# Optimization experiments

Measured on AMD Instinct MI355X. Metric: run time of the kernel, lower is better.

## Reference

```python
import jax, jax.numpy as jnp
import numpy as np

R, S, H, B = 50000, 8, 128, 4096

def setup_inputs() -> dict:
    key = jax.random.key(0)
    ks = jax.random.split(key, 8)
    return {
        "memory": jax.random.normal(ks[0], (R, S, H), dtype=jnp.float32) * 0.02,
        "o_emb_w": jax.random.normal(ks[1], (H,), dtype=jnp.float32),
        "o_emb_r": jax.random.normal(ks[2], (B, H), dtype=jnp.float32),
        "attn_W": jax.random.normal(ks[3], (H, H), dtype=jnp.float32) * (1.0 / np.sqrt(H)),
        "sim_w": jax.random.normal(ks[4], (2 * H, 1), dtype=jnp.float32) * 0.05,
        "sim_b": jax.random.normal(ks[5], (1,), dtype=jnp.float32) * 0.05,
        "forget_w": jax.random.normal(ks[6], (2 * H, 1), dtype=jnp.float32) * 0.05,
        "o_rg": 12345,
        "d_rg": jax.random.randint(ks[7], (B,), 0, R, dtype=jnp.int32),
    }

def reference(memory, o_emb_w, o_emb_r, attn_W, sim_w, sim_b, forget_w, o_rg, d_rg):
    h = memory.shape[-1]
    # --- write (state='w'): gather one region, sigmoid forget gate, scatter update ---
    sel = memory[o_rg]                                   # [S, H]
    o_ext = jnp.broadcast_to(o_emb_w, sel.shape)         # [S, H]
    # forget_linear(cat([o_emb, mem])) with no bias
    gate = jax.nn.sigmoid(o_ext @ forget_w[:h] + sel @ forget_w[h:])  # [S, 1]
    new_slot = sel * (1.0 - gate) + o_ext * gate
    new_mem = memory.at[o_rg].set(new_slot)              # equivalent to memory*(1-pad)+o_emb*pad
    # --- read (state='r'): gather per-batch region, concat-MLP attention over slots ---
    km = new_mem[d_rg]                                   # [B, S, H]
    q = o_emb_r @ attn_W                                 # [B, H]
    kv = km @ attn_W                                     # [B, S, H] (key == value input, same projection)
    # sim_mlp = Linear(2H,1)+ReLU applied to cat([q, k]), then softmax over slot dim
    logits = jax.nn.relu((q @ sim_w[:h])[:, None, :] + kv @ sim_w[h:] + sim_b)  # [B, S, 1]
    score = jax.nn.softmax(logits, axis=-2)              # softmax over slots
    mem_out = jnp.sum(score * kv, axis=-2)               # [B, H]
    return mem_out
```

## Files before the change

### kernel.cpp

```cpp
#include <hip/hip_runtime.h>
#include <math.h>

#define H 128
#define S 8
#define BB 4

__device__ __forceinline__ float wave_allreduce_sum(float v) {
    #pragma unroll
    for (int off = 32; off; off >>= 1) v += __shfl_xor(v, off, 64);
    return v;
}

__global__ __launch_bounds__(128) void prep_kernel(
        const float* __restrict__ memory,
        const float* __restrict__ o_emb_w,
        const float* __restrict__ attn_W,
        const float* __restrict__ sim_w,
        const float* __restrict__ forget_w,
        const int*   __restrict__ o_rg_p,
        float* __restrict__ ws) {
    const int t = threadIdx.x;
    float a1 = 0.f, a2 = 0.f;
    const float* wrow = attn_W + t * H;
    #pragma unroll 4
    for (int j = 0; j < H; ++j) {
        float w = wrow[j];
        a1 += w * sim_w[j];
        a2 += w * sim_w[H + j];
    }
    ws[t]     = a1;
    ws[H + t] = a2;

    __shared__ float red[9][H];
    __shared__ float gate[S];
    __shared__ float dow_s;
    const int o_rg = o_rg_p[0];
    const float* sel = memory + (size_t)o_rg * (S * H);
    red[0][t] = o_emb_w[t] * forget_w[t];
    #pragma unroll
    for (int s = 0; s < S; ++s) red[1 + s][t] = sel[s * H + t] * forget_w[H + t];
    __syncthreads();
    if (t < 9) {
        float sum = 0.f;
        for (int i = 0; i < H; ++i) sum += red[t][i];
        if (t == 0) dow_s = sum; else red[t][0] = sum;
    }
    __syncthreads();
    if (t < S) gate[t] = 1.f / (1.f + expf(-(dow_s + red[1 + t][0])));
    __syncthreads();
    #pragma unroll
    for (int s = 0; s < S; ++s) {
        float g = gate[s];
        ws[2 * H + s * H + t] = sel[s * H + t] * (1.f - g) + o_emb_w[t] * g;
    }
}

__global__ __launch_bounds__(256) void main_kernel(
        const float* __restrict__ memory,
        const float* __restrict__ o_emb_r,
        const float* __restrict__ attn_W,
        const float* __restrict__ sim_b,
        const int*   __restrict__ o_rg_p,
        const int*   __restrict__ d_rg,
        const float* __restrict__ ws,
        float* __restrict__ out) {
    __shared__ float wm_lds[BB][H];
    const int u  = threadIdx.x;
    const int wv = u >> 6;
    const int L  = u & 63;
    const int b  = blockIdx.x * BB + wv;

    const int o_rg = o_rg_p[0];
    const int r    = d_rg[b];
    const float2* src = (r == o_rg)
        ? (const float2*)(ws + 2 * H)
        : (const float2*)(memory + (size_t)r * (S * H));

    float2 rows[S];
    #pragma unroll
    for (int s = 0; s < S; ++s) rows[s] = src[s * (H / 2) + L];

    const float2 vv1 = ((const float2*)ws)[L];
    const float2 vv2 = ((const float2*)(ws + H))[L];
    const float2 oe  = ((const float2*)o_emb_r)[(size_t)b * (H / 2) + L];

    const float qs = wave_allreduce_sum(oe.x * vv1.x + oe.y * vv1.y);
    float d2[S];
    #pragma unroll
    for (int s = 0; s < S; ++s)
        d2[s] = wave_allreduce_sum(rows[s].x * vv2.x + rows[s].y * vv2.y);

    const float sb = sim_b[0];
    float l[S], m = -INFINITY;
    #pragma unroll
    for (int s = 0; s < S; ++s) { l[s] = fmaxf(qs + d2[s] + sb, 0.f); m = fmaxf(m, l[s]); }
    float p[S], psum = 0.f;
    #pragma unroll
    for (int s = 0; s < S; ++s) { p[s] = expf(l[s] - m); psum += p[s]; }
    const float inv = 1.f / psum;

    float2 wm = {0.f, 0.f};
    #pragma unroll
    for (int s = 0; s < S; ++s) {
        float ps = p[s] * inv;
        wm.x += ps * rows[s].x;
        wm.y += ps * rows[s].y;
    }
    wm_lds[wv][2 * L]     = wm.x;
    wm_lds[wv][2 * L + 1] = wm.y;
    __syncthreads();

    const float2* W2 = (const float2*)attn_W;
    const float* wmrow = wm_lds[wv];
    float2 acc = {0.f, 0.f};
    #pragma unroll 4
    for (int i = 0; i < H; ++i) {
        float2 w  = W2[i * (H / 2) + L];
        float  wv_ = wmrow[i];
        acc.x += wv_ * w.x;
        acc.y += wv_ * w.y;
    }
    ((float2*)out)[(size_t)b * (H / 2) + L] = acc;
}

extern "C" void kernel_launch(void* const* d_in, const int* in_sizes, int n_in,
                              void* d_out, int out_size, void* d_ws, size_t ws_size,
                              hipStream_t stream) {
    const float* memory   = (const float*)d_in[0];
    const float* o_emb_w  = (const float*)d_in[1];
    const float* o_emb_r  = (const float*)d_in[2];
    const float* attn_W   = (const float*)d_in[3];
    const float* sim_w    = (const float*)d_in[4];
    const float* sim_b    = (const float*)d_in[5];
    const float* forget_w = (const float*)d_in[6];
    const int*   o_rg     = (const int*)d_in[7];
    const int*   d_rg     = (const int*)d_in[8];
    float* out = (float*)d_out;
    float* ws  = (float*)d_ws;

    const int B = in_sizes[8];

    prep_kernel<<<1, 128, 0, stream>>>(memory, o_emb_w, attn_W, sim_w, forget_w, o_rg, ws);
    main_kernel<<<B / BB, 256, 0, stream>>>(memory, o_emb_r, attn_W, sim_b, o_rg, d_rg, ws, out);
}
```

Baseline: 273.8 us.

## Fuse prep kernel into main kernel, recomputing projections and gate per block

Removes the single-block prep kernel and its workspace round trip. Each block now computes attn_W·sim_w vectors into shared memory itself, and any wave whose region equals o_rg applies the forget-gate update in registers. This drops a serialized launch and the one-block dependency, at the cost of redundant per-block matvec work (each block rereads all of attn_W) and an extra block-wide barrier.

```diff
diff --git a/kernel.cpp b/kernel.cpp
--- a/kernel.cpp
+++ b/kernel.cpp
@@ -1,70 +1,30 @@
 #include <hip/hip_runtime.h>
 #include <math.h>
 
-#define H 128
-#define S 8
+#define H  128
+#define S  8
 #define BB 4
 
-__device__ __forceinline__ float wave_allreduce_sum(float v) {
+__device__ __forceinline__ float wave_sum(float v) {
     #pragma unroll
     for (int off = 32; off; off >>= 1) v += __shfl_xor(v, off, 64);
     return v;
 }
 
-__global__ __launch_bounds__(128) void prep_kernel(
+__global__ __launch_bounds__(256) void fused_kernel(
         const float* __restrict__ memory,
         const float* __restrict__ o_emb_w,
+        const float* __restrict__ o_emb_r,
         const float* __restrict__ attn_W,
         const float* __restrict__ sim_w,
+        const float* __restrict__ sim_b,
         const float* __restrict__ forget_w,
         const int*   __restrict__ o_rg_p,
-        float* __restrict__ ws) {
-    const int t = threadIdx.x;
-    float a1 = 0.f, a2 = 0.f;
-    const float* wrow = attn_W + t * H;
-    #pragma unroll 4
-    for (int j = 0; j < H; ++j) {
-        float w = wrow[j];
-        a1 += w * sim_w[j];
-        a2 += w * sim_w[H + j];
-    }
-    ws[t]     = a1;
-    ws[H + t] = a2;
+        const int*   __restrict__ d_rg,
+        float* __restrict__ out) {
+    __shared__ float v1s[H], v2s[H];
+    __shared__ float wm_lds[BB][H];
 
-    __shared__ float red[9][H];
-    __shared__ float gate[S];
-    __shared__ float dow_s;
-    const int o_rg = o_rg_p[0];
-    const float* sel = memory + (size_t)o_rg * (S * H);
-    red[0][t] = o_emb_w[t] * forget_w[t];
-    #pragma unroll
-    for (int s = 0; s < S; ++s) red[1 + s][t] = sel[s * H + t] * forget_w[H + t];
-    __syncthreads();
-    if (t < 9) {
-        float sum = 0.f;
-        for (int i = 0; i < H; ++i) sum += red[t][i];
-        if (t == 0) dow_s = sum; else red[t][0] = sum;
-    }
-    __syncthreads();
-    if (t < S) gate[t] = 1.f / (1.f + expf(-(dow_s + red[1 + t][0])));
-    __syncthreads();
-    #pragma unroll
-    for (int s = 0; s < S; ++s) {
-        float g = gate[s];
-        ws[2 * H + s * H + t] = sel[s * H + t] * (1.f - g) + o_emb_w[t] * g;
-    }
-}
-
-__global__ __launch_bounds__(256) void main_kernel(
-        const float* __restrict__ memory,
-        const float* __restrict__ o_emb_r,
-        const float* __restrict__ attn_W,
-        const float* __restrict__ sim_b,
-        const int*   __restrict__ o_rg_p,
-        const int*   __restrict__ d_rg,
-        const float* __restrict__ ws,
-        float* __restrict__ out) {
-    __shared__ float wm_lds[BB][H];
     const int u  = threadIdx.x;
     const int wv = u >> 6;
     const int L  = u & 63;
@@ -72,23 +32,52 @@
 
     const int o_rg = o_rg_p[0];
     const int r    = d_rg[b];
-    const float2* src = (r == o_rg)
-        ? (const float2*)(ws + 2 * H)
-        : (const float2*)(memory + (size_t)r * (S * H));
 
+    const float2* src = (const float2*)(memory + (size_t)r * (S * H));
     float2 rows[S];
     #pragma unroll
     for (int s = 0; s < S; ++s) rows[s] = src[s * (H / 2) + L];
+    const float2 oe = ((const float2*)o_emb_r)[(size_t)b * (H / 2) + L];
 
-    const float2 vv1 = ((const float2*)ws)[L];
-    const float2 vv2 = ((const float2*)(ws + H))[L];
-    const float2 oe  = ((const float2*)o_emb_r)[(size_t)b * (H / 2) + L];
+    {
+        const int row = u & 127, half = u >> 7;
+        const float2* wr = (const float2*)(attn_W + row * H + half * 64);
+        const float2* s1 = (const float2*)(sim_w + half * 64);
+        const float2* s2 = (const float2*)(sim_w + H + half * 64);
+        float a1 = 0.f, a2 = 0.f;
+        #pragma unroll 8
+        for (int j = 0; j < 32; ++j) {
+            float2 w = wr[j], x1 = s1[j], x2 = s2[j];
+            a1 += w.x * x1.x + w.y * x1.y;
+            a2 += w.x * x2.x + w.y * x2.y;
+        }
+        if (half == 0) { v1s[row] = a1; v2s[row] = a2; }
+        __syncthreads();
+        if (half == 1) { v1s[row] += a1; v2s[row] += a2; }
+        __syncthreads();
+    }
 
-    const float qs = wave_allreduce_sum(oe.x * vv1.x + oe.y * vv1.y);
+    if (r == o_rg) {
+        const float2 ow = ((const float2*)o_emb_w)[L];
+        const float2 f1 = ((const float2*)forget_w)[L];
+        const float2 f2 = ((const float2*)(forget_w + H))[L];
+        const float base = wave_sum(ow.x * f1.x + ow.y * f1.y);
+        #pragma unroll
+        for (int s = 0; s < S; ++s) {
+            float d = wave_sum(rows[s].x * f2.x + rows[s].y * f2.y);
+            float g = 1.f / (1.f + expf(-(base + d)));
+            rows[s].x = rows[s].x * (1.f - g) + ow.x * g;
+            rows[s].y = rows[s].y * (1.f - g) + ow.y * g;
+        }
+    }
+
+    const float2 vv1 = ((const float2*)v1s)[L];
+    const float2 vv2 = ((const float2*)v2s)[L];
+    const float qs = wave_sum(oe.x * vv1.x + oe.y * vv1.y);
     float d2[S];
     #pragma unroll
     for (int s = 0; s < S; ++s)
-        d2[s] = wave_allreduce_sum(rows[s].x * vv2.x + rows[s].y * vv2.y);
+        d2[s] = wave_sum(rows[s].x * vv2.x + rows[s].y * vv2.y);
 
     const float sb = sim_b[0];
     float l[S], m = -INFINITY;
@@ -115,10 +104,10 @@
     float2 acc = {0.f, 0.f};
     #pragma unroll 4
     for (int i = 0; i < H; ++i) {
-        float2 w  = W2[i * (H / 2) + L];
-        float  wv_ = wmrow[i];
-        acc.x += wv_ * w.x;
-        acc.y += wv_ * w.y;
+        float2 w = W2[i * (H / 2) + L];
+        float  x = wmrow[i];
+        acc.x += x * w.x;
+        acc.y += x * w.y;
     }
     ((float2*)out)[(size_t)b * (H / 2) + L] = acc;
 }
@@ -136,10 +125,9 @@
     const int*   o_rg     = (const int*)d_in[7];
     const int*   d_rg     = (const int*)d_in[8];
     float* out = (float*)d_out;
-    float* ws  = (float*)d_ws;
 
     const int B = in_sizes[8];
 
-    prep_kernel<<<1, 128, 0, stream>>>(memory, o_emb_w, attn_W, sim_w, forget_w, o_rg, ws);
-    main_kernel<<<B / BB, 256, 0, stream>>>(memory, o_emb_r, attn_W, sim_b, o_rg, d_rg, ws, out);
+    fused_kernel<<<B / BB, 256, 0, stream>>>(
+        memory, o_emb_w, o_emb_r, attn_W, sim_w, sim_b, forget_w, o_rg, d_rg, out);
 }
```

New measurement: 271.7 us. About the same (-0.8%).
